# Performance work log

Hardware: AMD Instinct MI355X
Metric: run time of the kernel (lower is better)

The kernel has to match this reference:

```python
import jax, jax.numpy as jnp
import numpy as np

N_NODES = 50000
N_EDGES = 800000
IN_DIM = 128
HID = 64
HEADS = 4
OUT_DIM = 64
NEG_SLOPE = 0.2


def setup_inputs() -> dict:
    key = jax.random.key(0)
    ks = jax.random.split(key, 12)
    x = jax.random.normal(ks[0], (N_NODES, IN_DIM), dtype=jnp.float32)
    edge_index = jax.random.randint(ks[1], (2, N_EDGES), 0, N_NODES, dtype=jnp.int64)
    s = 0.1
    # GATConv layer 1: in_dim -> hid per head, 4 heads, concat
    W1 = jax.random.normal(ks[2], (IN_DIM, HEADS * HID), dtype=jnp.float32) * s
    a_src1 = jax.random.normal(ks[3], (HEADS, HID), dtype=jnp.float32) * s
    a_dst1 = jax.random.normal(ks[4], (HEADS, HID), dtype=jnp.float32) * s
    b1 = jnp.zeros((HEADS * HID,), dtype=jnp.float32)
    # GATConv layer 2: hid*heads -> out_dim, 1 head
    W2 = jax.random.normal(ks[5], (HEADS * HID, OUT_DIM), dtype=jnp.float32) * s
    a_src2 = jax.random.normal(ks[6], (1, OUT_DIM), dtype=jnp.float32) * s
    a_dst2 = jax.random.normal(ks[7], (1, OUT_DIM), dtype=jnp.float32) * s
    b2 = jnp.zeros((OUT_DIM,), dtype=jnp.float32)
    # final linear out_dim -> 1
    fc_w = jax.random.normal(ks[8], (OUT_DIM, 1), dtype=jnp.float32) * s
    fc_b = jnp.zeros((1,), dtype=jnp.float32)
    return {"x": x, "edge_index": edge_index, "W1": W1, "a_src1": a_src1,
            "a_dst1": a_dst1, "b1": b1, "W2": W2, "a_src2": a_src2,
            "a_dst2": a_dst2, "b2": b2, "fc_w": fc_w, "fc_b": fc_b}


def _gat_layer(x, src, dst, W, a_src, a_dst, bias, heads, out_c):
    """PyG-style GATConv: gather, edge attention, segment softmax, scatter-sum."""
    n = x.shape[0]
    h = (x @ W).reshape(n, heads, out_c)                    # [N,H,C]
    alpha_s = jnp.sum(h * a_src, axis=-1)                   # [N,H]
    alpha_d = jnp.sum(h * a_dst, axis=-1)                   # [N,H]
    e = jax.nn.leaky_relu(alpha_s[src] + alpha_d[dst], NEG_SLOPE)  # [E,H]
    # segment softmax over incoming edges of each destination node
    m = jax.ops.segment_max(e, dst, num_segments=n)         # [N,H]
    ex = jnp.exp(e - m[dst])
    den = jax.ops.segment_sum(ex, dst, num_segments=n)      # [N,H]
    alpha = ex / (den[dst] + 1e-16)                         # [E,H]
    out = jax.ops.segment_sum(alpha[:, :, None] * h[src], dst, num_segments=n)
    return out.reshape(n, heads * out_c) + bias


def reference(x, edge_index, W1, a_src1, a_dst1, b1, W2, a_src2, a_dst2, b2, fc_w, fc_b):
    n = x.shape[0]
    # GATConv default add_self_loops=True
    loop = jnp.arange(n, dtype=edge_index.dtype)
    src = jnp.concatenate([edge_index[0], loop])
    dst = jnp.concatenate([edge_index[1], loop])
    h = _gat_layer(x, src, dst, W1, a_src1, a_dst1, b1, HEADS, HID)
    h = jax.nn.elu(h)
    h = _gat_layer(h, src, dst, W2, a_src2, a_dst2, b2, 1, OUT_DIM)
    return jnp.squeeze(h @ fc_w + fc_b)                      # [N]
```

## Files before the change

### kernel.cpp

```cpp
#include <hip/hip_runtime.h>
#include <hip/hip_fp16.h>

#define N_NODES 50000
#define N_EDGES 800000
#define E_TOT   850000
#define IN_DIM  128
#define HID     64
#define HEADS   4
#define C1      256
#define OUT_DIM 64
#define NEG_SLOPE 0.2f

#define CP_NODES   32
#define CP_BLOCKS  ((N_NODES + CP_NODES - 1) / CP_NODES)
#define COUNT_BLOCKS ((E_TOT + 255) / 256)
#define NB_SCAN ((N_NODES + 255) / 256)

typedef __attribute__((ext_vector_type(8))) short v8s;
typedef __attribute__((ext_vector_type(4))) float v4f;

__device__ __forceinline__ unsigned int bf16_rne(float f) {
    unsigned int u = __float_as_uint(f);
    return (u + 0x7FFFu + ((u >> 16) & 1u)) >> 16;
}
__device__ __forceinline__ unsigned int bf16_pack2(float a, float b) {
    return bf16_rne(a) | (bf16_rne(b) << 16);
}
__device__ __forceinline__ float bf16_lo(unsigned int u) { return __uint_as_float(u << 16); }
__device__ __forceinline__ float bf16_hi(unsigned int u) { return __uint_as_float(u & 0xFFFF0000u); }

__device__ __forceinline__ unsigned int f16_pack2(float a, float b) {
    __half2 h = __floats2half2_rn(a, b);
    return *(unsigned int*)&h;
}
__device__ __forceinline__ float2 f16_unp2(unsigned int u) {
    __half2 h = *(__half2*)&u;
    return __half22float2(h);
}

__global__ __launch_bounds__(512) void prep_kernel(
    const float* __restrict__ W1, const float* __restrict__ a_src1,
    const float* __restrict__ a_dst1,
    const float* __restrict__ W2, const float* __restrict__ a_src2,
    const float* __restrict__ a_dst2, const float* __restrict__ b2,
    const float* __restrict__ fc_w, const float* __restrict__ fc_b,
    float* __restrict__ p_src, float* __restrict__ p_dst,
    float* __restrict__ v_s, float* __restrict__ v_d, float* __restrict__ v_z,
    float* __restrict__ cst, unsigned int* __restrict__ W1b)
{
    const int t = threadIdx.x;
    if (blockIdx.x > 0) {
        int idx = (blockIdx.x - 1) * 512 + t;
        int i    = idx & 3;
        int lane = (idx >> 2) & 63;
        int kk   = (idx >> 8) & 3;
        int nt   = (idx >> 10) & 3;
        int hh   = idx >> 12;
        int k0 = kk * 32 + (lane >> 4) * 8 + i * 2;
        int c  = hh * 64 + nt * 16 + (lane & 15);
        W1b[idx] = bf16_pack2(W1[(size_t)k0 * C1 + c], W1[(size_t)(k0 + 1) * C1 + c]);
        return;
    }
    const int k = t >> 2, h = t & 3;
    const float* wrow = W1 + k * C1 + h * HID;
    const float* as = a_src1 + h * HID;
    const float* ad = a_dst1 + h * HID;
    float s = 0.f, d = 0.f;
    for (int c = 0; c < HID; c++) {
        float w = wrow[c];
        s = fmaf(w, as[c], s);
        d = fmaf(w, ad[c], d);
    }
    p_src[k * HEADS + h] = s;
    p_dst[k * HEADS + h] = d;

    if (t < C1) {
        const float* w2row = W2 + t * OUT_DIM;
        float vs = 0.f, vd = 0.f, vz = 0.f;
        for (int c = 0; c < OUT_DIM; c++) {
            float w = w2row[c];
            vs = fmaf(w, a_src2[c], vs);
            vd = fmaf(w, a_dst2[c], vd);
            vz = fmaf(w, fc_w[c], vz);
        }
        v_s[t] = vs; v_d[t] = vd; v_z[t] = vz;
    }
    if (t == 0) {
        float s2 = 0.f;
        for (int c = 0; c < OUT_DIM; c++) s2 = fmaf(b2[c], fc_w[c], s2);
        cst[0] = s2 + fc_b[0];
    }
}

__global__ __launch_bounds__(256) void convproj_count_kernel(
    const float* __restrict__ x, const float* __restrict__ p_src,
    const float* __restrict__ p_dst, const int* __restrict__ dst_a,
    float* __restrict__ as1, float* __restrict__ ad1,
    unsigned int* __restrict__ xb, int* __restrict__ deg,
    int* __restrict__ posE)
{
    if (blockIdx.x >= CP_BLOCKS) {
        int j = (blockIdx.x - CP_BLOCKS) * 256 + threadIdx.x;
        if (j < E_TOT) {
            int d = (j < N_EDGES) ? dst_a[j] : (j - N_EDGES);
            posE[j] = atomicAdd(&deg[d], 1);
        }
        return;
    }
    __shared__ float ps[IN_DIM * HEADS];
    __shared__ float pd[IN_DIM * HEADS];
    const int t = threadIdx.x;
    for (int i = t; i < IN_DIM * HEADS; i += 256) { ps[i] = p_src[i]; pd[i] = p_dst[i]; }
    __syncthreads();
    const int wv   = t >> 6;
    const int lane = t & 63;
    float4 p0 = *(const float4*)(ps + (lane * 2) * HEADS);
    float4 p1 = *(const float4*)(ps + (lane * 2 + 1) * HEADS);
    float4 q0 = *(const float4*)(pd + (lane * 2) * HEADS);
    float4 q1 = *(const float4*)(pd + (lane * 2 + 1) * HEADS);
    const int nodeBase = blockIdx.x * CP_NODES + wv * 8;
    #pragma unroll
    for (int i = 0; i < 8; i++) {
        const int node = nodeBase + i;
        if (node >= N_NODES) break;
        float2 xv = *(const float2*)(x + (size_t)node * IN_DIM + lane * 2);
        xb[(size_t)node * 64 + lane] = bf16_pack2(xv.x, xv.y);
        float s0 = xv.x * p0.x + xv.y * p1.x;
        float s1 = xv.x * p0.y + xv.y * p1.y;
        float s2 = xv.x * p0.z + xv.y * p1.z;
        float s3 = xv.x * p0.w + xv.y * p1.w;
        float d0 = xv.x * q0.x + xv.y * q1.x;
        float d1 = xv.x * q0.y + xv.y * q1.y;
        float d2 = xv.x * q0.z + xv.y * q1.z;
        float d3 = xv.x * q0.w + xv.y * q1.w;
        #pragma unroll
        for (int off = 32; off; off >>= 1) {
            s0 += __shfl_down(s0, off, 64); s1 += __shfl_down(s1, off, 64);
            s2 += __shfl_down(s2, off, 64); s3 += __shfl_down(s3, off, 64);
            d0 += __shfl_down(d0, off, 64); d1 += __shfl_down(d1, off, 64);
            d2 += __shfl_down(d2, off, 64); d3 += __shfl_down(d3, off, 64);
        }
        if (lane == 0) {
            float4 sv = {s0, s1, s2, s3};
            float4 dv = {d0, d1, d2, d3};
            *(float4*)(as1 + node * 4) = sv;
            *(float4*)(ad1 + node * 4) = dv;
        }
    }
}

__global__ __launch_bounds__(256) void scanfuse_kernel(
    const int* __restrict__ deg, int* __restrict__ rowptr,
    int* aggP, int* incP)
{
    __shared__ int ps[256];
    __shared__ int bs[256];
    __shared__ int sprev;
    const int t = threadIdx.x;
    const int b = blockIdx.x;
    int i = b * 256 + t;
    int v = (i < N_NODES) ? deg[i] : 0;
    ps[t] = v;
    __syncthreads();
    for (int off = 1; off < 256; off <<= 1) {
        int u = (t >= off) ? ps[t - off] : 0;
        __syncthreads();
        ps[t] += u;
        __syncthreads();
    }
    if (t == 255) atomicExch(&aggP[b], ps[255] + 1);
    if (b == 0) {
        int val = 0;
        if (t < NB_SCAN) {
            while ((val = atomicAdd(&aggP[t], 0)) == 0) {}
            val -= 1;
        }
        bs[t] = (t < NB_SCAN) ? val : 0;
        __syncthreads();
        for (int off = 1; off < 256; off <<= 1) {
            int u = (t >= off) ? bs[t - off] : 0;
            __syncthreads();
            bs[t] += u;
            __syncthreads();
        }
        if (t < NB_SCAN) atomicExch(&incP[t], (bs[t] - val) + 1);
    }
    if (t == 0) {
        int val;
        while ((val = atomicAdd(&incP[b], 0)) == 0) {}
        sprev = val - 1;
    }
    __syncthreads();
    if (i <= N_NODES) rowptr[i] = sprev + ps[t] - v;
}

__global__ void fillw3_kernel(const int* __restrict__ src_a, const int* __restrict__ dst_a,
                              const int* __restrict__ rowptr, const int* __restrict__ posE,
                              const float* __restrict__ as1, const float* __restrict__ ad1,
                              int4* __restrict__ rec)
{
    int j = blockIdx.x * blockDim.x + threadIdx.x;
    if (j >= E_TOT) return;
    int s, d;
    if (j < N_EDGES) { s = src_a[j]; d = dst_a[j]; }
    else             { s = j - N_EDGES; d = s; }
    int slot = rowptr[d] + posE[j];
    float4 A  = *(const float4*)(as1 + s * 4);
    float4 Dv = *(const float4*)(ad1 + d * 4);
    float a0 = A.x + Dv.x, a1 = A.y + Dv.y, a2 = A.z + Dv.z, a3 = A.w + Dv.w;
    a0 = a0 > 0.f ? a0 : NEG_SLOPE * a0;
    a1 = a1 > 0.f ? a1 : NEG_SLOPE * a1;
    a2 = a2 > 0.f ? a2 : NEG_SLOPE * a2;
    a3 = a3 > 0.f ? a3 : NEG_SLOPE * a3;
    int4 r;
    r.x = s;
    r.y = (int)f16_pack2(__expf(a0), __expf(a1));
    r.z = (int)f16_pack2(__expf(a2), __expf(a3));
    r.w = 0;
    rec[slot] = r;
}

__global__ __launch_bounds__(256, 6) void agg1mlp_kernel(
    const int* __restrict__ rowptr, const int4* __restrict__ rec,
    const unsigned int* __restrict__ xb,
    const unsigned int* __restrict__ W1b, const float* __restrict__ b1,
    const float* __restrict__ v_s, const float* __restrict__ v_d,
    const float* __restrict__ v_z,
    float2* __restrict__ az, float* __restrict__ ad2)
{
    __shared__ unsigned int xsh[16 * 260];
    __shared__ float pr[4 * 16 * 3];
    const int t = threadIdx.x;
    const int nodeBase = blockIdx.x * 16;
    const int wv   = t >> 6;
    const int lane = t & 63;

    #pragma unroll 1
    for (int i = 0; i < 4; i++) {
        const int ln = wv * 4 + i;
        const int n  = nodeBase + ln;
        const int e0 = rowptr[n], e1 = rowptr[n + 1];

        float2 acc0 = {0,0}, acc1 = {0,0}, acc2 = {0,0}, acc3 = {0,0};
        float den0 = 0, den1 = 0, den2 = 0, den3 = 0;
        int e = e0;
        int4 R0, R1, R2, R3;
        if (e + 4 <= e1) {
            R0 = rec[e]; R1 = rec[e + 1]; R2 = rec[e + 2]; R3 = rec[e + 3];
        }
        while (e + 4 <= e1) {
            unsigned int xu0 = xb[(size_t)R0.x * 64 + lane];
            unsigned int xu1 = xb[(size_t)R1.x * 64 + lane];
            unsigned int xu2 = xb[(size_t)R2.x * 64 + lane];
            unsigned int xu3 = xb[(size_t)R3.x * 64 + lane];
            unsigned int wy0 = R0.y, wz0 = R0.z, wy1 = R1.y, wz1 = R1.z;
            unsigned int wy2 = R2.y, wz2 = R2.z, wy3 = R3.y, wz3 = R3.z;
            e += 4;
            if (e + 4 <= e1) {
                R0 = rec[e]; R1 = rec[e + 1]; R2 = rec[e + 2]; R3 = rec[e + 3];
            }
            float2 W0a = f16_unp2(wy0), W0b = f16_unp2(wz0);
            float2 W1a = f16_unp2(wy1), W1b_ = f16_unp2(wz1);
            float2 W2a = f16_unp2(wy2), W2b = f16_unp2(wz2);
            float2 W3a = f16_unp2(wy3), W3b = f16_unp2(wz3);
            float a0 = bf16_lo(xu0), b0 = bf16_hi(xu0);
            float a1 = bf16_lo(xu1), b1v = bf16_hi(xu1);
            float a2 = bf16_lo(xu2), b2v = bf16_hi(xu2);
            float a3 = bf16_lo(xu3), b3v = bf16_hi(xu3);
            acc0.x = fmaf(W0a.x, a0, acc0.x); acc0.y = fmaf(W0a.x, b0, acc0.y);
            acc1.x = fmaf(W0a.y, a0, acc1.x); acc1.y = fmaf(W0a.y, b0, acc1.y);
            acc2.x = fmaf(W0b.x, a0, acc2.x); acc2.y = fmaf(W0b.x, b0, acc2.y);
            acc3.x = fmaf(W0b.y, a0, acc3.x); acc3.y = fmaf(W0b.y, b0, acc3.y);
            acc0.x = fmaf(W1a.x, a1, acc0.x); acc0.y = fmaf(W1a.x, b1v, acc0.y);
            acc1.x = fmaf(W1a.y, a1, acc1.x); acc1.y = fmaf(W1a.y, b1v, acc1.y);
            acc2.x = fmaf(W1b_.x, a1, acc2.x); acc2.y = fmaf(W1b_.x, b1v, acc2.y);
            acc3.x = fmaf(W1b_.y, a1, acc3.x); acc3.y = fmaf(W1b_.y, b1v, acc3.y);
            acc0.x = fmaf(W2a.x, a2, acc0.x); acc0.y = fmaf(W2a.x, b2v, acc0.y);
            acc1.x = fmaf(W2a.y, a2, acc1.x); acc1.y = fmaf(W2a.y, b2v, acc1.y);
            acc2.x = fmaf(W2b.x, a2, acc2.x); acc2.y = fmaf(W2b.x, b2v, acc2.y);
            acc3.x = fmaf(W2b.y, a2, acc3.x); acc3.y = fmaf(W2b.y, b2v, acc3.y);
            acc0.x = fmaf(W3a.x, a3, acc0.x); acc0.y = fmaf(W3a.x, b3v, acc0.y);
            acc1.x = fmaf(W3a.y, a3, acc1.x); acc1.y = fmaf(W3a.y, b3v, acc1.y);
            acc2.x = fmaf(W3b.x, a3, acc2.x); acc2.y = fmaf(W3b.x, b3v, acc2.y);
            acc3.x = fmaf(W3b.y, a3, acc3.x); acc3.y = fmaf(W3b.y, b3v, acc3.y);
            den0 += (W0a.x + W1a.x) + (W2a.x + W3a.x);
            den1 += (W0a.y + W1a.y) + (W2a.y + W3a.y);
            den2 += (W0b.x + W1b_.x) + (W2b.x + W3b.x);
            den3 += (W0b.y + W1b_.y) + (W2b.y + W3b.y);
        }
        for (; e < e1; e++) {
            int4 r0 = rec[e];
            unsigned int xu = xb[(size_t)r0.x * 64 + lane];
            float2 Wa = f16_unp2(r0.y), Wb = f16_unp2(r0.z);
            float xa = bf16_lo(xu), xbv = bf16_hi(xu);
            acc0.x = fmaf(Wa.x, xa, acc0.x); acc0.y = fmaf(Wa.x, xbv, acc0.y);
            acc1.x = fmaf(Wa.y, xa, acc1.x); acc1.y = fmaf(Wa.y, xbv, acc1.y);
            acc2.x = fmaf(Wb.x, xa, acc2.x); acc2.y = fmaf(Wb.x, xbv, acc2.y);
            acc3.x = fmaf(Wb.y, xa, acc3.x); acc3.y = fmaf(Wb.y, xbv, acc3.y);
            den0 += Wa.x; den1 += Wa.y; den2 += Wb.x; den3 += Wb.y;
        }
        float i0 = 1.f / (den0 + 1e-16f), i1 = 1.f / (den1 + 1e-16f);
        float i2 = 1.f / (den2 + 1e-16f), i3 = 1.f / (den3 + 1e-16f);
        unsigned int* o = xsh + ln * 260 + lane;
        o[0 * 64] = bf16_pack2(acc0.x * i0, acc0.y * i0);
        o[1 * 64] = bf16_pack2(acc1.x * i1, acc1.y * i1);
        o[2 * 64] = bf16_pack2(acc2.x * i2, acc2.y * i2);
        o[3 * 64] = bf16_pack2(acc3.x * i3, acc3.y * i3);
    }
    __syncthreads();

    {
        const int h = wv;
        const int m = lane & 15, quad = lane >> 4;
        const unsigned int* abase = xsh + m * 260 + h * 64 + quad * 4;
        v8s af0 = *(const v8s*)(abase + 0);
        v8s af1 = *(const v8s*)(abase + 16);
        v8s af2 = *(const v8s*)(abase + 32);
        v8s af3 = *(const v8s*)(abase + 48);

        float Sr[4] = {0,0,0,0}, Dr[4] = {0,0,0,0}, Zr[4] = {0,0,0,0};
        #pragma unroll
        for (int nt = 0; nt < 4; nt++) {
            const unsigned int* bbase = W1b + (size_t)(h * 16 + nt * 4) * 256 + lane * 4;
            v4f acc = {0.f, 0.f, 0.f, 0.f};
            acc = __builtin_amdgcn_mfma_f32_16x16x32_bf16(af0, *(const v8s*)(bbase + 0 * 256), acc, 0, 0, 0);
            acc = __builtin_amdgcn_mfma_f32_16x16x32_bf16(af1, *(const v8s*)(bbase + 1 * 256), acc, 0, 0, 0);
            acc = __builtin_amdgcn_mfma_f32_16x16x32_bf16(af2, *(const v8s*)(bbase + 2 * 256), acc, 0, 0, 0);
            acc = __builtin_amdgcn_mfma_f32_16x16x32_bf16(af3, *(const v8s*)(bbase + 3 * 256), acc, 0, 0, 0);
            const int c = h * 64 + nt * 16 + m;
            float bb = b1[c], vsc = v_s[c], vdc = v_d[c], vzc = v_z[c];
            #pragma unroll
            for (int r = 0; r < 4; r++) {
                float o = acc[r] + bb;
                o = o > 0.f ? o : __expf(o) - 1.f;
                Sr[r] = fmaf(o, vsc, Sr[r]);
                Dr[r] = fmaf(o, vdc, Dr[r]);
                Zr[r] = fmaf(o, vzc, Zr[r]);
            }
        }
        #pragma unroll
        for (int off = 8; off; off >>= 1) {
            #pragma unroll
            for (int r = 0; r < 4; r++) {
                Sr[r] += __shfl_down(Sr[r], off, 16);
                Dr[r] += __shfl_down(Dr[r], off, 16);
                Zr[r] += __shfl_down(Zr[r], off, 16);
            }
        }
        if (m == 0) {
            #pragma unroll
            for (int r = 0; r < 4; r++) {
                const int row = quad * 4 + r;
                pr[(h * 16 + row) * 3 + 0] = Sr[r];
                pr[(h * 16 + row) * 3 + 1] = Dr[r];
                pr[(h * 16 + row) * 3 + 2] = Zr[r];
            }
        }
    }
    __syncthreads();

    if (t < 16) {
        float s = 0.f, d = 0.f, z = 0.f;
        #pragma unroll
        for (int w = 0; w < 4; w++) {
            s += pr[(w * 16 + t) * 3 + 0];
            d += pr[(w * 16 + t) * 3 + 1];
            z += pr[(w * 16 + t) * 3 + 2];
        }
        const int node = nodeBase + t;
        float2 azv = {s, z};
        az[node]  = azv;
        ad2[node] = d;
    }
}

__global__ __launch_bounds__(256) void agg2z_kernel(
    const int* __restrict__ rowptr, const int4* __restrict__ rec,
    const float2* __restrict__ az, const float* __restrict__ ad2,
    const float* __restrict__ cst, float* __restrict__ out)
{
    int gid  = blockIdx.x * blockDim.x + threadIdx.x;
    int n    = gid >> 3;
    int sl   = threadIdx.x & 7;
    if (n >= N_NODES) return;
    const float adh = ad2[n];
    const int e0 = rowptr[n], e1 = rowptr[n + 1];

    float acc = 0.f, den = 0.f;
    for (int e = e0 + sl; e < e1; e += 8) {
        int s = rec[e].x;
        float2 v = az[s];
        float a = v.x + adh;
        a = a > 0.f ? a : NEG_SLOPE * a;
        float w = __expf(a);
        acc = fmaf(w, v.y, acc);
        den += w;
    }
    #pragma unroll
    for (int off = 4; off; off >>= 1) {
        acc += __shfl_down(acc, off, 8);
        den += __shfl_down(den, off, 8);
    }
    if (sl == 0) out[n] = acc / (den + 1e-16f) + cst[0];
}

extern "C" void kernel_launch(void* const* d_in, const int* in_sizes, int n_in,
                              void* d_out, int out_size, void* d_ws, size_t ws_size,
                              hipStream_t stream)
{
    const float* x      = (const float*)d_in[0];
    const int*   ei     = (const int*)d_in[1];
    const float* W1     = (const float*)d_in[2];
    const float* a_src1 = (const float*)d_in[3];
    const float* a_dst1 = (const float*)d_in[4];
    const float* b1     = (const float*)d_in[5];
    const float* W2     = (const float*)d_in[6];
    const float* a_src2 = (const float*)d_in[7];
    const float* a_dst2 = (const float*)d_in[8];
    const float* b2     = (const float*)d_in[9];
    const float* fc_w   = (const float*)d_in[10];
    const float* fc_b   = (const float*)d_in[11];
    float* out = (float*)d_out;

    const int* srcA = ei;
    const int* dstA = ei + N_EDGES;

    float* ws = (float*)d_ws;
    size_t off = 0;
    unsigned int* xb    = (unsigned int*)(ws + off); off += (size_t)N_NODES * 64;
    int4* rec      = (int4*)(ws + off); off += (size_t)E_TOT * 4 + 256;
    int* posE      = (int*)(ws + off); off += E_TOT + 256;
    float* as1     = ws + off; off += (size_t)N_NODES * HEADS;
    float* ad1     = ws + off; off += (size_t)N_NODES * HEADS;
    float2* az     = (float2*)(ws + off); off += (size_t)N_NODES * 2;
    float* ad2     = ws + off; off += N_NODES;
    float* p_src   = ws + off; off += IN_DIM * HEADS;
    float* p_dst   = ws + off; off += IN_DIM * HEADS;
    float* v_s     = ws + off; off += C1;
    float* v_d     = ws + off; off += C1;
    float* v_z     = ws + off; off += C1;
    float* cst     = ws + off; off += 2;
    unsigned int* W1b = (unsigned int*)(ws + off); off += 16384;
    int* rowptr    = (int*)(ws + off); off += N_NODES + 1 + 256;
    int* aggP      = (int*)(ws + off); off += 256;
    int* incP      = (int*)(ws + off); off += 256;
    int* deg       = (int*)(ws + off); off += N_NODES;
    hipMemsetAsync(aggP, 0, (512 + N_NODES) * sizeof(int), stream);

    prep_kernel<<<33, 512, 0, stream>>>(W1, a_src1, a_dst1, W2, a_src2, a_dst2,
                                        b2, fc_w, fc_b, p_src, p_dst, v_s, v_d, v_z, cst, W1b);

    convproj_count_kernel<<<CP_BLOCKS + COUNT_BLOCKS, 256, 0, stream>>>(
        x, p_src, p_dst, dstA, as1, ad1, xb, deg, posE);

    scanfuse_kernel<<<NB_SCAN, 256, 0, stream>>>(deg, rowptr, aggP, incP);

    fillw3_kernel<<<COUNT_BLOCKS, 256, 0, stream>>>(srcA, dstA, rowptr, posE,
                                                    as1, ad1, rec);

    agg1mlp_kernel<<<N_NODES / 16, 256, 0, stream>>>(rowptr, rec, xb, W1b, b1,
                                                     v_s, v_d, v_z, az, ad2);

    agg2z_kernel<<<(N_NODES * 8 + 255) / 256, 256, 0, stream>>>(rowptr, rec, az, ad2, cst, out);
}
```

Before: 247.1 us.

## Split edge records into SoA src/fp32 weights and use persistent tile scheduler

The packed int4 edge record (src plus fp16 weights) becomes two arrays: an int source index and fp32 float4 attention weights. The layer-1 aggregation kernel turns into a persistent grid of 2048 blocks that take 16-node tiles from an atomic counter, and its occupancy hint drops from 6 to 4. The explicit register prefetch of the next records is removed. Layer-2 aggregation now reads only the compact src array, but fp32 weights double the weight traffic in layer 1 and the manual prefetch is lost.

```diff
diff --git a/kernel.cpp b/kernel.cpp
--- a/kernel.cpp
+++ b/kernel.cpp
@@ -10,6 +10,7 @@
 #define C1      256
 #define OUT_DIM 64
 #define NEG_SLOPE 0.2f
+#define N_TILES (N_NODES / 16)
 
 #define CP_NODES   32
 #define CP_BLOCKS  ((N_NODES + CP_NODES - 1) / CP_NODES)
@@ -28,15 +29,6 @@
 }
 __device__ __forceinline__ float bf16_lo(unsigned int u) { return __uint_as_float(u << 16); }
 __device__ __forceinline__ float bf16_hi(unsigned int u) { return __uint_as_float(u & 0xFFFF0000u); }
-
-__device__ __forceinline__ unsigned int f16_pack2(float a, float b) {
-    __half2 h = __floats2half2_rn(a, b);
-    return *(unsigned int*)&h;
-}
-__device__ __forceinline__ float2 f16_unp2(unsigned int u) {
-    __half2 h = *(__half2*)&u;
-    return __half22float2(h);
-}
 
 __global__ __launch_bounds__(512) void prep_kernel(
     const float* __restrict__ W1, const float* __restrict__ a_src1,
@@ -197,7 +189,7 @@
 __global__ void fillw3_kernel(const int* __restrict__ src_a, const int* __restrict__ dst_a,
                               const int* __restrict__ rowptr, const int* __restrict__ posE,
                               const float* __restrict__ as1, const float* __restrict__ ad1,
-                              int4* __restrict__ rec)
+                              int* __restrict__ srcs, float4* __restrict__ w4)
 {
     int j = blockIdx.x * blockDim.x + threadIdx.x;
     if (j >= E_TOT) return;
@@ -212,170 +204,166 @@
     a1 = a1 > 0.f ? a1 : NEG_SLOPE * a1;
     a2 = a2 > 0.f ? a2 : NEG_SLOPE * a2;
     a3 = a3 > 0.f ? a3 : NEG_SLOPE * a3;
-    int4 r;
-    r.x = s;
-    r.y = (int)f16_pack2(__expf(a0), __expf(a1));
-    r.z = (int)f16_pack2(__expf(a2), __expf(a3));
-    r.w = 0;
-    rec[slot] = r;
-}
-
-__global__ __launch_bounds__(256, 6) void agg1mlp_kernel(
-    const int* __restrict__ rowptr, const int4* __restrict__ rec,
+    srcs[slot] = s;
+    float4 w = {__expf(a0), __expf(a1), __expf(a2), __expf(a3)};
+    w4[slot] = w;
+}
+
+__global__ __launch_bounds__(256, 4) void agg1mlp_kernel(
+    const int* __restrict__ rowptr, const int* __restrict__ srcs,
+    const float4* __restrict__ w4,
     const unsigned int* __restrict__ xb,
     const unsigned int* __restrict__ W1b, const float* __restrict__ b1,
     const float* __restrict__ v_s, const float* __restrict__ v_d,
     const float* __restrict__ v_z,
-    float2* __restrict__ az, float* __restrict__ ad2)
+    float2* __restrict__ az, float* __restrict__ ad2, int* __restrict__ tctr)
 {
     __shared__ unsigned int xsh[16 * 260];
     __shared__ float pr[4 * 16 * 3];
+    __shared__ int stile;
     const int t = threadIdx.x;
-    const int nodeBase = blockIdx.x * 16;
     const int wv   = t >> 6;
     const int lane = t & 63;
 
-    #pragma unroll 1
-    for (int i = 0; i < 4; i++) {
-        const int ln = wv * 4 + i;
-        const int n  = nodeBase + ln;
-        const int e0 = rowptr[n], e1 = rowptr[n + 1];
-
-        float2 acc0 = {0,0}, acc1 = {0,0}, acc2 = {0,0}, acc3 = {0,0};
-        float den0 = 0, den1 = 0, den2 = 0, den3 = 0;
-        int e = e0;
-        int4 R0, R1, R2, R3;
-        if (e + 4 <= e1) {
-            R0 = rec[e]; R1 = rec[e + 1]; R2 = rec[e + 2]; R3 = rec[e + 3];
-        }
-        while (e + 4 <= e1) {
-            unsigned int xu0 = xb[(size_t)R0.x * 64 + lane];
-            unsigned int xu1 = xb[(size_t)R1.x * 64 + lane];
-            unsigned int xu2 = xb[(size_t)R2.x * 64 + lane];
-            unsigned int xu3 = xb[(size_t)R3.x * 64 + lane];
-            unsigned int wy0 = R0.y, wz0 = R0.z, wy1 = R1.y, wz1 = R1.z;
-            unsigned int wy2 = R2.y, wz2 = R2.z, wy3 = R3.y, wz3 = R3.z;
-            e += 4;
-            if (e + 4 <= e1) {
-                R0 = rec[e]; R1 = rec[e + 1]; R2 = rec[e + 2]; R3 = rec[e + 3];
-            }
-            float2 W0a = f16_unp2(wy0), W0b = f16_unp2(wz0);
-            float2 W1a = f16_unp2(wy1), W1b_ = f16_unp2(wz1);
-            float2 W2a = f16_unp2(wy2), W2b = f16_unp2(wz2);
-            float2 W3a = f16_unp2(wy3), W3b = f16_unp2(wz3);
-            float a0 = bf16_lo(xu0), b0 = bf16_hi(xu0);
-            float a1 = bf16_lo(xu1), b1v = bf16_hi(xu1);
-            float a2 = bf16_lo(xu2), b2v = bf16_hi(xu2);
-            float a3 = bf16_lo(xu3), b3v = bf16_hi(xu3);
-            acc0.x = fmaf(W0a.x, a0, acc0.x); acc0.y = fmaf(W0a.x, b0, acc0.y);
-            acc1.x = fmaf(W0a.y, a0, acc1.x); acc1.y = fmaf(W0a.y, b0, acc1.y);
-            acc2.x = fmaf(W0b.x, a0, acc2.x); acc2.y = fmaf(W0b.x, b0, acc2.y);
-            acc3.x = fmaf(W0b.y, a0, acc3.x); acc3.y = fmaf(W0b.y, b0, acc3.y);
-            acc0.x = fmaf(W1a.x, a1, acc0.x); acc0.y = fmaf(W1a.x, b1v, acc0.y);
-            acc1.x = fmaf(W1a.y, a1, acc1.x); acc1.y = fmaf(W1a.y, b1v, acc1.y);
-            acc2.x = fmaf(W1b_.x, a1, acc2.x); acc2.y = fmaf(W1b_.x, b1v, acc2.y);
-            acc3.x = fmaf(W1b_.y, a1, acc3.x); acc3.y = fmaf(W1b_.y, b1v, acc3.y);
-            acc0.x = fmaf(W2a.x, a2, acc0.x); acc0.y = fmaf(W2a.x, b2v, acc0.y);
-            acc1.x = fmaf(W2a.y, a2, acc1.x); acc1.y = fmaf(W2a.y, b2v, acc1.y);
-            acc2.x = fmaf(W2b.x, a2, acc2.x); acc2.y = fmaf(W2b.x, b2v, acc2.y);
-            acc3.x = fmaf(W2b.y, a2, acc3.x); acc3.y = fmaf(W2b.y, b2v, acc3.y);
-            acc0.x = fmaf(W3a.x, a3, acc0.x); acc0.y = fmaf(W3a.x, b3v, acc0.y);
-            acc1.x = fmaf(W3a.y, a3, acc1.x); acc1.y = fmaf(W3a.y, b3v, acc1.y);
-            acc2.x = fmaf(W3b.x, a3, acc2.x); acc2.y = fmaf(W3b.x, b3v, acc2.y);
-            acc3.x = fmaf(W3b.y, a3, acc3.x); acc3.y = fmaf(W3b.y, b3v, acc3.y);
-            den0 += (W0a.x + W1a.x) + (W2a.x + W3a.x);
-            den1 += (W0a.y + W1a.y) + (W2a.y + W3a.y);
-            den2 += (W0b.x + W1b_.x) + (W2b.x + W3b.x);
-            den3 += (W0b.y + W1b_.y) + (W2b.y + W3b.y);
-        }
-        for (; e < e1; e++) {
-            int4 r0 = rec[e];
-            unsigned int xu = xb[(size_t)r0.x * 64 + lane];
-            float2 Wa = f16_unp2(r0.y), Wb = f16_unp2(r0.z);
-            float xa = bf16_lo(xu), xbv = bf16_hi(xu);
-            acc0.x = fmaf(Wa.x, xa, acc0.x); acc0.y = fmaf(Wa.x, xbv, acc0.y);
-            acc1.x = fmaf(Wa.y, xa, acc1.x); acc1.y = fmaf(Wa.y, xbv, acc1.y);
-            acc2.x = fmaf(Wb.x, xa, acc2.x); acc2.y = fmaf(Wb.x, xbv, acc2.y);
-            acc3.x = fmaf(Wb.y, xa, acc3.x); acc3.y = fmaf(Wb.y, xbv, acc3.y);
-            den0 += Wa.x; den1 += Wa.y; den2 += Wb.x; den3 += Wb.y;
-        }
-        float i0 = 1.f / (den0 + 1e-16f), i1 = 1.f / (den1 + 1e-16f);
-        float i2 = 1.f / (den2 + 1e-16f), i3 = 1.f / (den3 + 1e-16f);
-        unsigned int* o = xsh + ln * 260 + lane;
-        o[0 * 64] = bf16_pack2(acc0.x * i0, acc0.y * i0);
-        o[1 * 64] = bf16_pack2(acc1.x * i1, acc1.y * i1);
-        o[2 * 64] = bf16_pack2(acc2.x * i2, acc2.y * i2);
-        o[3 * 64] = bf16_pack2(acc3.x * i3, acc3.y * i3);
-    }
-    __syncthreads();
-
-    {
-        const int h = wv;
-        const int m = lane & 15, quad = lane >> 4;
-        const unsigned int* abase = xsh + m * 260 + h * 64 + quad * 4;
-        v8s af0 = *(const v8s*)(abase + 0);
-        v8s af1 = *(const v8s*)(abase + 16);
-        v8s af2 = *(const v8s*)(abase + 32);
-        v8s af3 = *(const v8s*)(abase + 48);
-
-        float Sr[4] = {0,0,0,0}, Dr[4] = {0,0,0,0}, Zr[4] = {0,0,0,0};
-        #pragma unroll
-        for (int nt = 0; nt < 4; nt++) {
-            const unsigned int* bbase = W1b + (size_t)(h * 16 + nt * 4) * 256 + lane * 4;
-            v4f acc = {0.f, 0.f, 0.f, 0.f};
-            acc = __builtin_amdgcn_mfma_f32_16x16x32_bf16(af0, *(const v8s*)(bbase + 0 * 256), acc, 0, 0, 0);
-            acc = __builtin_amdgcn_mfma_f32_16x16x32_bf16(af1, *(const v8s*)(bbase + 1 * 256), acc, 0, 0, 0);
-            acc = __builtin_amdgcn_mfma_f32_16x16x32_bf16(af2, *(const v8s*)(bbase + 2 * 256), acc, 0, 0, 0);
-            acc = __builtin_amdgcn_mfma_f32_16x16x32_bf16(af3, *(const v8s*)(bbase + 3 * 256), acc, 0, 0, 0);
-            const int c = h * 64 + nt * 16 + m;
-            float bb = b1[c], vsc = v_s[c], vdc = v_d[c], vzc = v_z[c];
+    for (;;) {
+        if (t == 0) stile = atomicAdd(tctr, 1);
+        __syncthreads();
+        const int tile = stile;
+        if (tile >= N_TILES) break;
+        const int nodeBase = tile * 16;
+
+        #pragma unroll 1
+        for (int i = 0; i < 4; i++) {
+            const int ln = wv * 4 + i;
+            const int n  = nodeBase + ln;
+            const int e0 = rowptr[n], e1 = rowptr[n + 1];
+
+            float2 acc0 = {0,0}, acc1 = {0,0}, acc2 = {0,0}, acc3 = {0,0};
+            float den0 = 0, den1 = 0, den2 = 0, den3 = 0;
+            int e = e0;
+            for (; e + 4 <= e1; e += 4) {
+                int s0 = srcs[e], s1 = srcs[e + 1];
+                int s2 = srcs[e + 2], s3 = srcs[e + 3];
+                float4 W0 = w4[e],     W1v = w4[e + 1];
+                float4 W2 = w4[e + 2], W3v = w4[e + 3];
+                unsigned int xu0 = xb[(unsigned)(s0 << 6) + lane];
+                unsigned int xu1 = xb[(unsigned)(s1 << 6) + lane];
+                unsigned int xu2 = xb[(unsigned)(s2 << 6) + lane];
+                unsigned int xu3 = xb[(unsigned)(s3 << 6) + lane];
+                float a0 = bf16_lo(xu0), b0 = bf16_hi(xu0);
+                float a1 = bf16_lo(xu1), b1v = bf16_hi(xu1);
+                float a2 = bf16_lo(xu2), b2v = bf16_hi(xu2);
+                float a3 = bf16_lo(xu3), b3v = bf16_hi(xu3);
+                acc0.x = fmaf(W0.x, a0, acc0.x); acc0.y = fmaf(W0.x, b0, acc0.y);
+                acc1.x = fmaf(W0.y, a0, acc1.x); acc1.y = fmaf(W0.y, b0, acc1.y);
+                acc2.x = fmaf(W0.z, a0, acc2.x); acc2.y = fmaf(W0.z, b0, acc2.y);
+                acc3.x = fmaf(W0.w, a0, acc3.x); acc3.y = fmaf(W0.w, b0, acc3.y);
+                acc0.x = fmaf(W1v.x, a1, acc0.x); acc0.y = fmaf(W1v.x, b1v, acc0.y);
+                acc1.x = fmaf(W1v.y, a1, acc1.x); acc1.y = fmaf(W1v.y, b1v, acc1.y);
+                acc2.x = fmaf(W1v.z, a1, acc2.x); acc2.y = fmaf(W1v.z, b1v, acc2.y);
+                acc3.x = fmaf(W1v.w, a1, acc3.x); acc3.y = fmaf(W1v.w, b1v, acc3.y);
+                acc0.x = fmaf(W2.x, a2, acc0.x); acc0.y = fmaf(W2.x, b2v, acc0.y);
+                acc1.x = fmaf(W2.y, a2, acc1.x); acc1.y = fmaf(W2.y, b2v, acc1.y);
+                acc2.x = fmaf(W2.z, a2, acc2.x); acc2.y = fmaf(W2.z, b2v, acc2.y);
+                acc3.x = fmaf(W2.w, a2, acc3.x); acc3.y = fmaf(W2.w, b2v, acc3.y);
+                acc0.x = fmaf(W3v.x, a3, acc0.x); acc0.y = fmaf(W3v.x, b3v, acc0.y);
+                acc1.x = fmaf(W3v.y, a3, acc1.x); acc1.y = fmaf(W3v.y, b3v, acc1.y);
+                acc2.x = fmaf(W3v.z, a3, acc2.x); acc2.y = fmaf(W3v.z, b3v, acc2.y);
+                acc3.x = fmaf(W3v.w, a3, acc3.x); acc3.y = fmaf(W3v.w, b3v, acc3.y);
+                den0 += (W0.x + W1v.x) + (W2.x + W3v.x);
+                den1 += (W0.y + W1v.y) + (W2.y + W3v.y);
+                den2 += (W0.z + W1v.z) + (W2.z + W3v.z);
+                den3 += (W0.w + W1v.w) + (W2.w + W3v.w);
+            }
+            for (; e < e1; e++) {
+                int s0 = srcs[e];
+                float4 W0 = w4[e];
+                unsigned int xu = xb[(unsigned)(s0 << 6) + lane];
+                float xa = bf16_lo(xu), xbv = bf16_hi(xu);
+                acc0.x = fmaf(W0.x, xa, acc0.x); acc0.y = fmaf(W0.x, xbv, acc0.y);
+                acc1.x = fmaf(W0.y, xa, acc1.x); acc1.y = fmaf(W0.y, xbv, acc1.y);
+                acc2.x = fmaf(W0.z, xa, acc2.x); acc2.y = fmaf(W0.z, xbv, acc2.y);
+                acc3.x = fmaf(W0.w, xa, acc3.x); acc3.y = fmaf(W0.w, xbv, acc3.y);
+                den0 += W0.x; den1 += W0.y; den2 += W0.z; den3 += W0.w;
+            }
+            float i0 = 1.f / (den0 + 1e-16f), i1 = 1.f / (den1 + 1e-16f);
+            float i2 = 1.f / (den2 + 1e-16f), i3 = 1.f / (den3 + 1e-16f);
+            unsigned int* o = xsh + ln * 260 + lane;
+            o[0 * 64] = bf16_pack2(acc0.x * i0, acc0.y * i0);
+            o[1 * 64] = bf16_pack2(acc1.x * i1, acc1.y * i1);
+            o[2 * 64] = bf16_pack2(acc2.x * i2, acc2.y * i2);
+            o[3 * 64] = bf16_pack2(acc3.x * i3, acc3.y * i3);
+        }
+        __syncthreads();
+
+        {
+            const int h = wv;
+            const int m = lane & 15, quad = lane >> 4;
+            const unsigned int* abase = xsh + m * 260 + h * 64 + quad * 4;
+            v8s af0 = *(const v8s*)(abase + 0);
+            v8s af1 = *(const v8s*)(abase + 16);
+            v8s af2 = *(const v8s*)(abase + 32);
+            v8s af3 = *(const v8s*)(abase + 48);
+
+            float Sr[4] = {0,0,0,0}, Dr[4] = {0,0,0,0}, Zr[4] = {0,0,0,0};
             #pragma unroll
-            for (int r = 0; r < 4; r++) {
-                float o = acc[r] + bb;
-                o = o > 0.f ? o : __expf(o) - 1.f;
-                Sr[r] = fmaf(o, vsc, Sr[r]);
-                Dr[r] = fmaf(o, vdc, Dr[r]);
-                Zr[r] = fmaf(o, vzc, Zr[r]);
-            }
-        }
-        #pragma unroll
-        for (int off = 8; off; off >>= 1) {
+            for (int nt = 0; nt < 4; nt++) {
+                const unsigned int* bbase = W1b + (size_t)(h * 16 + nt * 4) * 256 + lane * 4;
+                v4f acc = {0.f, 0.f, 0.f, 0.f};
+                acc = __builtin_amdgcn_mfma_f32_16x16x32_bf16(af0, *(const v8s*)(bbase + 0 * 256), acc, 0, 0, 0);
+                acc = __builtin_amdgcn_mfma_f32_16x16x32_bf16(af1, *(const v8s*)(bbase + 1 * 256), acc, 0, 0, 0);
+                acc = __builtin_amdgcn_mfma_f32_16x16x32_bf16(af2, *(const v8s*)(bbase + 2 * 256), acc, 0, 0, 0);
+                acc = __builtin_amdgcn_mfma_f32_16x16x32_bf16(af3, *(const v8s*)(bbase + 3 * 256), acc, 0, 0, 0);
+                const int c = h * 64 + nt * 16 + m;
+                float bb = b1[c], vsc = v_s[c], vdc = v_d[c], vzc = v_z[c];
+                #pragma unroll
+                for (int r = 0; r < 4; r++) {
+                    float o = acc[r] + bb;
+                    o = o > 0.f ? o : __expf(o) - 1.f;
+                    Sr[r] = fmaf(o, vsc, Sr[r]);
+                    Dr[r] = fmaf(o, vdc, Dr[r]);
+                    Zr[r] = fmaf(o, vzc, Zr[r]);
+                }
+            }
             #pragma unroll
-            for (int r = 0; r < 4; r++) {
-                Sr[r] += __shfl_down(Sr[r], off, 16);
-                Dr[r] += __shfl_down(Dr[r], off, 16);
-                Zr[r] += __shfl_down(Zr[r], off, 16);
-            }
-        }
-        if (m == 0) {
+            for (int off = 8; off; off >>= 1) {
+                #pragma unroll
+                for (int r = 0; r < 4; r++) {
+                    Sr[r] += __shfl_down(Sr[r], off, 16);
+                    Dr[r] += __shfl_down(Dr[r], off, 16);
+                    Zr[r] += __shfl_down(Zr[r], off, 16);
+                }
+            }
+            if (m == 0) {
+                #pragma unroll
+                for (int r = 0; r < 4; r++) {
+                    const int row = quad * 4 + r;
+                    pr[(h * 16 + row) * 3 + 0] = Sr[r];
+                    pr[(h * 16 + row) * 3 + 1] = Dr[r];
+                    pr[(h * 16 + row) * 3 + 2] = Zr[r];
+                }
+            }
+        }
+        __syncthreads();
+
+        if (t < 16) {
+            float s = 0.f, d = 0.f, z = 0.f;
             #pragma unroll
-            for (int r = 0; r < 4; r++) {
-                const int row = quad * 4 + r;
-                pr[(h * 16 + row) * 3 + 0] = Sr[r];
-                pr[(h * 16 + row) * 3 + 1] = Dr[r];
-                pr[(h * 16 + row) * 3 + 2] = Zr[r];
-            }
-        }
-    }
-    __syncthreads();
-
-    if (t < 16) {
-        float s = 0.f, d = 0.f, z = 0.f;
-        #pragma unroll
-        for (int w = 0; w < 4; w++) {
-            s += pr[(w * 16 + t) * 3 + 0];
-            d += pr[(w * 16 + t) * 3 + 1];
-            z += pr[(w * 16 + t) * 3 + 2];
-        }
-        const int node = nodeBase + t;
-        float2 azv = {s, z};
-        az[node]  = azv;
-        ad2[node] = d;
+            for (int w = 0; w < 4; w++) {
+                s += pr[(w * 16 + t) * 3 + 0];
+                d += pr[(w * 16 + t) * 3 + 1];
+                z += pr[(w * 16 + t) * 3 + 2];
+            }
+            const int node = nodeBase + t;
+            float2 azv = {s, z};
+            az[node]  = azv;
+            ad2[node] = d;
+        }
     }
 }
 
 __global__ __launch_bounds__(256) void agg2z_kernel(
-    const int* __restrict__ rowptr, const int4* __restrict__ rec,
+    const int* __restrict__ rowptr, const int* __restrict__ srcs,
     const float2* __restrict__ az, const float* __restrict__ ad2,
     const float* __restrict__ cst, float* __restrict__ out)
 {
@@ -388,7 +376,7 @@
 
     float acc = 0.f, den = 0.f;
     for (int e = e0 + sl; e < e1; e += 8) {
-        int s = rec[e].x;
+        int s = srcs[e];
         float2 v = az[s];
         float a = v.x + adh;
         a = a > 0.f ? a : NEG_SLOPE * a;
@@ -428,7 +416,8 @@
     float* ws = (float*)d_ws;
     size_t off = 0;
     unsigned int* xb    = (unsigned int*)(ws + off); off += (size_t)N_NODES * 64;
-    int4* rec      = (int4*)(ws + off); off += (size_t)E_TOT * 4 + 256;
+    float4* w4     = (float4*)(ws + off); off += (size_t)E_TOT * 4 + 256;
+    int* srcs      = (int*)(ws + off); off += E_TOT + 256;
     int* posE      = (int*)(ws + off); off += E_TOT + 256;
     float* as1     = ws + off; off += (size_t)N_NODES * HEADS;
     float* ad1     = ws + off; off += (size_t)N_NODES * HEADS;
@@ -444,8 +433,9 @@
     int* rowptr    = (int*)(ws + off); off += N_NODES + 1 + 256;
     int* aggP      = (int*)(ws + off); off += 256;
     int* incP      = (int*)(ws + off); off += 256;
+    int* tctr      = (int*)(ws + off); off += 256;
     int* deg       = (int*)(ws + off); off += N_NODES;
-    hipMemsetAsync(aggP, 0, (512 + N_NODES) * sizeof(int), stream);
+    hipMemsetAsync(aggP, 0, (768 + N_NODES) * sizeof(int), stream);
 
     prep_kernel<<<33, 512, 0, stream>>>(W1, a_src1, a_dst1, W2, a_src2, a_dst2,
                                         b2, fc_w, fc_b, p_src, p_dst, v_s, v_d, v_z, cst, W1b);
@@ -456,10 +446,10 @@
     scanfuse_kernel<<<NB_SCAN, 256, 0, stream>>>(deg, rowptr, aggP, incP);
 
     fillw3_kernel<<<COUNT_BLOCKS, 256, 0, stream>>>(srcA, dstA, rowptr, posE,
-                                                    as1, ad1, rec);
-
-    agg1mlp_kernel<<<N_NODES / 16, 256, 0, stream>>>(rowptr, rec, xb, W1b, b1,
-                                                     v_s, v_d, v_z, az, ad2);
-
-    agg2z_kernel<<<(N_NODES * 8 + 255) / 256, 256, 0, stream>>>(rowptr, rec, az, ad2, cst, out);
-}
+                                                    as1, ad1, srcs, w4);
+
+    agg1mlp_kernel<<<2048, 256, 0, stream>>>(rowptr, srcs, w4, xb, W1b, b1,
+                                             v_s, v_d, v_z, az, ad2, tctr);
+
+    agg2z_kernel<<<(N_NODES * 8 + 255) / 256, 256, 0, stream>>>(rowptr, srcs, az, ad2, cst, out);
+}
```

Result: slower. 295.8 us (+19.7%).
